# Performance work log

Measured on AMD Instinct MI355X. Metric: run time of the kernel, lower is better.

Reference implementation:

```python
import jax, jax.numpy as jnp
import numpy as np
from jax import lax

HEADS = 8
DK = 128
DV = 128  # attention_channels


def circ_conv(x, w):
    # Conv2d with circular padding that preserves spatial size (odd kernel).
    k = w.shape[2]
    p = k // 2
    if p > 0:
        x = jnp.pad(x, ((0, 0), (0, 0), (p, p), (p, p)), mode='wrap')
    return lax.conv_general_dilated(x, w, (1, 1), 'VALID',
                                    dimension_numbers=('NCHW', 'OIHW', 'NCHW'))


def setup_inputs() -> dict:
    key = jax.random.key(0)
    k1, k2, k3, k4 = jax.random.split(key, 4)
    x = jax.random.normal(k1, (4, 128, 48, 48), dtype=jnp.float32)
    w_init = jax.random.normal(k2, (128, 128, 3, 3), dtype=jnp.float32) * 0.03
    w_qkv = jax.random.normal(k3, (384, 128, 3, 3), dtype=jnp.float32) * 0.03
    w_out = jax.random.normal(k4, (128, 128, 1, 1), dtype=jnp.float32) * 0.1
    return {"x": x, "w_init": w_init, "w_qkv": w_qkv, "w_out": w_out}


def reference(x, w_init, w_qkv, w_out):
    out = circ_conv(x, w_init)               # (b, out_ch - dv, h, w)
    b, _, H, W = out.shape
    N = H * W
    dk_h = DK // HEADS
    dv_h = DV // HEADS

    qkv = circ_conv(x, w_qkv)                # (b, 2*dk+dv, h, w)
    q, k, v = jnp.split(qkv, [DK, 2 * DK], axis=1)

    scale = dk_h ** (-0.5)
    fq = q.reshape(b, HEADS, dk_h, N) * scale
    fk = k.reshape(b, HEADS, dk_h, N)
    fv = v.reshape(b, HEADS, dv_h, N)

    logits = jnp.einsum('bhdn,bhdm->bhnm', fq, fk)     # (b,H,N,N)
    weights = jax.nn.softmax(logits, axis=-1)
    attn = jnp.einsum('bhnm,bhdm->bhnd', weights, fv)  # (b,H,N,dv_h)

    # Faithful to torch: raw reshape (b,H,N,dv_h) -> (b,H,dv_h,h,w)
    attn = attn.reshape(b, HEADS, dv_h, H, W)
    attn = attn.reshape(b, HEADS * dv_h, H, W)
    attn = circ_conv(attn, w_out)
    return jnp.concatenate([out, attn], axis=1)
```

## Files before the change

### kernel.cpp

```cpp
#include <hip/hip_runtime.h>

typedef __attribute__((ext_vector_type(8))) short short8;
typedef __attribute__((ext_vector_type(4))) short shortx4;
typedef __attribute__((ext_vector_type(4))) float floatx4;
typedef __attribute__((ext_vector_type(4))) _Float16 half4;
typedef __attribute__((ext_vector_type(2))) _Float16 half2v;

__device__ __forceinline__ short bf16_short(float f) {
    unsigned u = __builtin_bit_cast(unsigned, f);
    u = (u + 0x7fff + ((u >> 16) & 1)) >> 16;
    return (short)u;
}

__device__ __forceinline__ float fast_exp2(float x) {
#if __has_builtin(__builtin_amdgcn_exp2f)
    return __builtin_amdgcn_exp2f(x);
#else
    return __expf(x * 0.6931471805599453f);
#endif
}

__device__ __forceinline__ half4 pk4(float p0, float p1, float p2, float p3) {
#if __has_builtin(__builtin_amdgcn_cvt_pkrtz)
    half2v lo = __builtin_bit_cast(half2v, __builtin_amdgcn_cvt_pkrtz(p0, p1));
    half2v hi = __builtin_bit_cast(half2v, __builtin_amdgcn_cvt_pkrtz(p2, p3));
    half4 o; o[0] = lo[0]; o[1] = lo[1]; o[2] = hi[0]; o[3] = hi[1];
    return o;
#else
    half4 o; o[0] = (_Float16)p0; o[1] = (_Float16)p1;
    o[2] = (_Float16)p2; o[3] = (_Float16)p3;
    return o;
#endif
}

__global__ __launch_bounds__(256) void transform_w(
    const float* __restrict__ wi, const float* __restrict__ wq,
    const float* __restrict__ wo, const float* __restrict__ x,
    short* __restrict__ Wt, short* __restrict__ Wot, short* __restrict__ Xt)
{
    if (blockIdx.x < 2368) {
        int idx = blockIdx.x * 256 + threadIdx.x;
        if (idx < 589824) {
            int j  = idx & 7;
            int t1 = idx >> 3;
            int co = t1 & 127;
            int t2 = t1 >> 7;
            int chunk = t2 & 15;
            int t3 = t2 >> 4;
            int cog = t3 & 3;
            int tap = t3 >> 2;
            int ci = chunk * 8 + j;
            float v;
            if (cog == 0) v = wi[(co * 128 + ci) * 9 + tap];
            else          v = wq[((((cog - 1) * 128) + co) * 128 + ci) * 9 + tap];
            Wt[idx] = bf16_short(v);
        } else {
            int i2 = idx - 589824;
            int j  = i2 & 7;
            int co = (i2 >> 3) & 127;
            int chunk = i2 >> 10;
            int ci = chunk * 8 + j;
            Wot[i2] = bf16_short(wo[co * 128 + ci]);
        }
    } else {
        int xid = (blockIdx.x - 2368) * 256 + threadIdx.x;
        int col   = xid % 48;
        int row   = (xid / 48) % 48;
        int chunk = (xid / 2304) % 16;
        int b     = xid / 36864;
        const float* xs = x + ((b * 128 + chunk * 8) * 48 + row) * 48 + col;
        short8 o;
        #pragma unroll
        for (int j = 0; j < 8; ++j) o[j] = bf16_short(xs[j * 2304]);
        *(short8*)&Xt[(size_t)xid * 8] = o;
    }
}

__global__ __launch_bounds__(256) void conv_main(
    const short* __restrict__ Xt, const short* __restrict__ Wt,
    float* __restrict__ dout, _Float16* __restrict__ qT,
    _Float16* __restrict__ kT, _Float16* __restrict__ vA)
{
    const int y   = blockIdx.x;
    const int cog = blockIdx.y;
    const int b   = blockIdx.z;

    __shared__ short Xs[16 * 3 * 48 * 8];

    const int t = threadIdx.x;
    const int wave = t >> 6, lane = t & 63, quad = lane >> 4, l16 = lane & 15;

    const short* wA = Wt + (size_t)cog * 16384 + (wave * 32 + l16) * 8;

    short8 A[2][8];
    #pragma unroll
    for (int kk = 0; kk < 4; ++kk) {
        int chA = kk * 4 + quad;
        A[0][kk * 2 + 0] = *(const short8*)(wA + chA * 1024);
        A[0][kk * 2 + 1] = *(const short8*)(wA + chA * 1024 + 128);
    }

    {
        const short* xtb = Xt + (size_t)b * 16 * 48 * 48 * 8;
        #pragma unroll
        for (int it = 0; it < 9; ++it) {
            int w     = it * 256 + t;
            int col   = w % 48;
            int row3  = (w / 48) % 3;
            int chunk = w / 144;
            int rowg  = y + row3 - 1;
            rowg = (rowg < 0) ? rowg + 48 : (rowg >= 48 ? rowg - 48 : rowg);
            short8 v = *(const short8*)&xtb[((chunk * 48 + rowg) * 48 + col) * 8];
            *(short8*)&Xs[((chunk * 3 + row3) * 48 + col) * 8] = v;
        }
    }

    floatx4 acc[2][3];
    #pragma unroll
    for (int i = 0; i < 2; ++i)
        #pragma unroll
        for (int jn = 0; jn < 3; ++jn) acc[i][jn] = (floatx4){0.f, 0.f, 0.f, 0.f};

    __syncthreads();

    #pragma unroll
    for (int tap = 0; tap < 9; ++tap) {
        const int cur = tap & 1;
        if (tap < 8) {
            const short* wn = wA + (tap + 1) * 65536;
            #pragma unroll
            for (int kk = 0; kk < 4; ++kk) {
                int chA = kk * 4 + quad;
                A[cur ^ 1][kk * 2 + 0] = *(const short8*)(wn + chA * 1024);
                A[cur ^ 1][kk * 2 + 1] = *(const short8*)(wn + chA * 1024 + 128);
            }
        }

        const int dy = tap / 3, dx = tap % 3;
        int colw[3];
        #pragma unroll
        for (int nt = 0; nt < 3; ++nt) {
            int c = nt * 16 + l16 + dx - 1;
            c = (c < 0) ? c + 48 : (c >= 48 ? c - 48 : c);
            colw[nt] = c;
        }

        #pragma unroll
        for (int kk = 0; kk < 4; ++kk) {
            int chA = kk * 4 + quad;
            short8 a0 = A[cur][kk * 2 + 0];
            short8 a1 = A[cur][kk * 2 + 1];
            #pragma unroll
            for (int nt = 0; nt < 3; ++nt) {
                short8 bf = *(const short8*)&Xs[((chA * 3 + dy) * 48 + colw[nt]) * 8];
                acc[0][nt] = __builtin_amdgcn_mfma_f32_16x16x32_bf16(a0, bf, acc[0][nt], 0, 0, 0);
                acc[1][nt] = __builtin_amdgcn_mfma_f32_16x16x32_bf16(a1, bf, acc[1][nt], 0, 0, 0);
            }
        }
    }

    if (cog == 0) {
        #pragma unroll
        for (int mt = 0; mt < 2; ++mt)
            #pragma unroll
            for (int nt = 0; nt < 3; ++nt)
                #pragma unroll
                for (int r = 0; r < 4; ++r) {
                    int n    = y * 48 + nt * 16 + l16;
                    int co_l = wave * 32 + mt * 16 + quad * 4 + r;
                    dout[(b * 256 + co_l) * 2304 + n] = acc[mt][nt][r];
                }
    } else if (cog == 3) {
        #pragma unroll
        for (int mt = 0; mt < 2; ++mt) {
            int hh = wave * 2 + mt;
            #pragma unroll
            for (int nt = 0; nt < 3; ++nt) {
                int s = y * 3 + nt;
                _Float16* dst = vA + (((size_t)(b * 8 + hh) * 144 + s) * 16) * 16 + l16;
                #pragma unroll
                for (int r = 0; r < 4; ++r)
                    dst[(quad * 4 + r) * 16] = (_Float16)acc[mt][nt][r];
            }
        }
    } else {
        _Float16* dst = (cog == 1) ? qT : kT;
        const float scale = (cog == 1) ? 0.360673762f : 1.0f;
        #pragma unroll
        for (int mt = 0; mt < 2; ++mt) {
            int hh = wave * 2 + mt;
            #pragma unroll
            for (int nt = 0; nt < 3; ++nt) {
                int n = y * 48 + nt * 16 + l16;
                half4 o;
                #pragma unroll
                for (int r = 0; r < 4; ++r) o[r] = (_Float16)(acc[mt][nt][r] * scale);
                *(half4*)&dst[((b * 8 + hh) * 2304 + n) * 16 + quad * 4] = o;
            }
        }
    }
}

__global__ __launch_bounds__(256) void attn_kernel(
    const _Float16* __restrict__ qT, const _Float16* __restrict__ kT,
    const _Float16* __restrict__ vA, short* __restrict__ attnbuf)
{
    const int bh = blockIdx.y;
    const int n0 = blockIdx.x * 64;

    __shared__ float Red[4][4][64][5];

    const int t = threadIdx.x;
    const int wave = t >> 6, lane = t & 63, quad = lane >> 4, l16 = lane & 15;

    const _Float16* qTb = qT + (size_t)bh * 2304 * 16;
    const _Float16* kTb = kT + (size_t)bh * 2304 * 16;
    const _Float16* vAb = vA + (size_t)bh * 144 * 256;

    half4 qf[4];
    #pragma unroll
    for (int f = 0; f < 4; ++f)
        qf[f] = *(const half4*)(qTb + (n0 + f * 16 + l16) * 16 + quad * 4);

    floatx4 accA[4], accB[4];
    float lsum[4];
    #pragma unroll
    for (int f = 0; f < 4; ++f) {
        accA[f] = (floatx4){0.f,0.f,0.f,0.f};
        accB[f] = (floatx4){0.f,0.f,0.f,0.f};
        lsum[f] = 0.f;
    }

    const int mbase = wave * 576;
    const int sig0  = wave * 36;
    const int vofs  = l16 * 16 + quad * 4;

    half4 kfA = *(const half4*)(kTb + (mbase + l16) * 16 + quad * 4);
    half4 vfA = *(const half4*)(vAb + sig0 * 256 + vofs);
    half4 kfB = *(const half4*)(kTb + (mbase + 16 + l16) * 16 + quad * 4);
    half4 vfB = *(const half4*)(vAb + (sig0 + 1) * 256 + vofs);

    #pragma unroll 2
    for (int s = 0; s < 18; ++s) {
        half4 kA = kfA, vAc = vfA, kB = kfB, vBc = vfB;
        if (s < 17) {
            int m1 = mbase + (s + 1) * 32;
            int sg = sig0 + (s + 1) * 2;
            kfA = *(const half4*)(kTb + (m1 + l16) * 16 + quad * 4);
            vfA = *(const half4*)(vAb + sg * 256 + vofs);
            kfB = *(const half4*)(kTb + (m1 + 16 + l16) * 16 + quad * 4);
            vfB = *(const half4*)(vAb + (sg + 1) * 256 + vofs);
        }
        floatx4 z = {0.f,0.f,0.f,0.f};
        floatx4 stA[4], stB[4];
        #pragma unroll
        for (int f = 0; f < 4; ++f)
            stA[f] = __builtin_amdgcn_mfma_f32_16x16x16f16(kA, qf[f], z, 0, 0, 0);
        #pragma unroll
        for (int f = 0; f < 4; ++f)
            stB[f] = __builtin_amdgcn_mfma_f32_16x16x16f16(kB, qf[f], z, 0, 0, 0);

        #pragma unroll
        for (int f = 0; f < 4; ++f) {
            float a0 = fast_exp2(stA[f][0]);
            float a1 = fast_exp2(stA[f][1]);
            float a2 = fast_exp2(stA[f][2]);
            float a3 = fast_exp2(stA[f][3]);
            lsum[f] += (a0 + a1) + (a2 + a3);
            accA[f] = __builtin_amdgcn_mfma_f32_16x16x16f16(vAc, pk4(a0,a1,a2,a3), accA[f], 0, 0, 0);
        }
        #pragma unroll
        for (int f = 0; f < 4; ++f) {
            float b0 = fast_exp2(stB[f][0]);
            float b1 = fast_exp2(stB[f][1]);
            float b2 = fast_exp2(stB[f][2]);
            float b3 = fast_exp2(stB[f][3]);
            lsum[f] += (b0 + b1) + (b2 + b3);
            accB[f] = __builtin_amdgcn_mfma_f32_16x16x16f16(vBc, pk4(b0,b1,b2,b3), accB[f], 0, 0, 0);
        }
    }

    #pragma unroll
    for (int f = 0; f < 4; ++f) {
        lsum[f] += __shfl_xor(lsum[f], 16, 64);
        lsum[f] += __shfl_xor(lsum[f], 32, 64);
    }

    #pragma unroll
    for (int f = 0; f < 4; ++f) {
        #pragma unroll
        for (int r = 0; r < 4; ++r) Red[wave][f][lane][r] = accA[f][r] + accB[f][r];
        Red[wave][f][lane][4] = lsum[f];
    }
    __syncthreads();

    {
        const int f = wave;
        float tot[4] = {0.f, 0.f, 0.f, 0.f};
        float ls = 0.f;
        #pragma unroll
        for (int w = 0; w < 4; ++w) {
            #pragma unroll
            for (int r = 0; r < 4; ++r) tot[r] += Red[w][f][lane][r];
            ls += Red[w][f][lane][4];
        }
        float rinv = 1.0f / ls;
        shortx4 o;
        #pragma unroll
        for (int r = 0; r < 4; ++r) o[r] = bf16_short(tot[r] * rinv);
        int n = n0 + f * 16 + l16;
        *(shortx4*)&attnbuf[((size_t)bh * 2304 + n) * 16 + quad * 4] = o;
    }
}

__global__ __launch_bounds__(256) void conv1x1(
    const short* __restrict__ attnbuf, const short* __restrict__ Wot,
    float* __restrict__ dout)
{
    const int b    = blockIdx.y;
    const int col0 = blockIdx.x * 32;
    constexpr int RSA = 136;

    __shared__ short Wo[16 * 128 * 8];
    __shared__ short As[32 * RSA];

    const int t = threadIdx.x;
    {
        short8* dst = (short8*)Wo;
        const short8* src = (const short8*)Wot;
        #pragma unroll
        for (int it = 0; it < 8; ++it) dst[it * 256 + t] = src[it * 256 + t];
    }
    {
        const short* ab = attnbuf + b * 128 * 2304;
        #pragma unroll
        for (int it = 0; it < 8; ++it) {
            int e = it * 256 + t;
            int ci = e >> 4, cp = e & 15;
            unsigned v = *(const unsigned*)(ab + ci * 2304 + col0 + cp * 2);
            As[(cp * 2) * RSA + ci]     = (short)(v & 0xffff);
            As[(cp * 2 + 1) * RSA + ci] = (short)(v >> 16);
        }
    }
    __syncthreads();

    const int wave = t >> 6, lane = t & 63, quad = lane >> 4, l16 = lane & 15;
    floatx4 acc[2][2];
    #pragma unroll
    for (int i = 0; i < 2; ++i)
        #pragma unroll
        for (int j = 0; j < 2; ++j) acc[i][j] = (floatx4){0.f, 0.f, 0.f, 0.f};

    #pragma unroll
    for (int kk = 0; kk < 4; ++kk) {
        int chA = kk * 4 + quad;
        short8 a0 = *(const short8*)&Wo[(chA * 128 + wave * 32 + l16) * 8];
        short8 a1 = *(const short8*)&Wo[(chA * 128 + wave * 32 + 16 + l16) * 8];
        #pragma unroll
        for (int nt = 0; nt < 2; ++nt) {
            short8 bf = *(const short8*)&As[(nt * 16 + l16) * RSA + kk * 32 + quad * 8];
            acc[0][nt] = __builtin_amdgcn_mfma_f32_16x16x32_bf16(a0, bf, acc[0][nt], 0, 0, 0);
            acc[1][nt] = __builtin_amdgcn_mfma_f32_16x16x32_bf16(a1, bf, acc[1][nt], 0, 0, 0);
        }
    }

    #pragma unroll
    for (int mt = 0; mt < 2; ++mt)
        #pragma unroll
        for (int nt = 0; nt < 2; ++nt)
            #pragma unroll
            for (int r = 0; r < 4; ++r) {
                int co  = wave * 32 + mt * 16 + quad * 4 + r;
                int col = col0 + nt * 16 + l16;
                dout[(b * 256 + 128 + co) * 2304 + col] = acc[mt][nt][r];
            }
}

extern "C" void kernel_launch(void* const* d_in, const int* in_sizes, int n_in,
                              void* d_out, int out_size, void* d_ws, size_t ws_size,
                              hipStream_t stream)
{
    const float* x  = (const float*)d_in[0];
    const float* wi = (const float*)d_in[1];
    const float* wq = (const float*)d_in[2];
    const float* wo = (const float*)d_in[3];
    float* dout = (float*)d_out;

    char* ws = (char*)d_ws;
    _Float16* qT   = (_Float16*)(ws);
    _Float16* kT   = (_Float16*)(ws + 2359296);
    _Float16* vA   = (_Float16*)(ws + 4718592);
    short* attnbuf = (short*)(ws + 7077888);
    short* Wt      = (short*)(ws + 9437184);
    short* Wot     = (short*)(ws + 10616832);
    short* Xt      = (short*)(ws + 10649600);

    transform_w<<<2944, 256, 0, stream>>>(wi, wq, wo, x, Wt, Wot, Xt);
    conv_main<<<dim3(48, 4, 4), 256, 0, stream>>>(Xt, Wt, dout, qT, kT, vA);
    attn_kernel<<<dim3(36, 32), 256, 0, stream>>>(qT, kT, vA, attnbuf);
    conv1x1<<<dim3(72, 4), 256, 0, stream>>>(attnbuf, Wot, dout);
}
```

Before: 121.5 us.

## Split conv K-reduction across two wave groups with LDS reduction

Doubles the conv_main block to 512 threads. Each half of the waves handles half of the input-channel chunks for every tap, and the partial accumulators are then summed through shared memory before the epilogue. The goal is more waves in flight per block and shorter per-wave MFMA chains, which should hide the weight-load latency better on a grid of only 768 blocks. In exchange it adds an LDS reduction with two extra barriers and leaves half the waves idle during the epilogue.

```diff
diff --git a/kernel.cpp b/kernel.cpp
--- a/kernel.cpp
+++ b/kernel.cpp
@@ -76,7 +76,7 @@
     }
 }
 
-__global__ __launch_bounds__(256) void conv_main(
+__global__ __launch_bounds__(512) void conv_main(
     const short* __restrict__ Xt, const short* __restrict__ Wt,
     float* __restrict__ dout, _Float16* __restrict__ qT,
     _Float16* __restrict__ kT, _Float16* __restrict__ vA)
@@ -89,13 +89,15 @@
 
     const int t = threadIdx.x;
     const int wave = t >> 6, lane = t & 63, quad = lane >> 4, l16 = lane & 15;
-
-    const short* wA = Wt + (size_t)cog * 16384 + (wave * 32 + l16) * 8;
-
-    short8 A[2][8];
-    #pragma unroll
-    for (int kk = 0; kk < 4; ++kk) {
-        int chA = kk * 4 + quad;
+    const int wv = wave & 3;
+    const int kk0 = (wave >> 2) * 2;
+
+    const short* wA = Wt + (size_t)cog * 16384 + (wv * 32 + l16) * 8;
+
+    short8 A[2][4];
+    #pragma unroll
+    for (int kk = 0; kk < 2; ++kk) {
+        int chA = (kk0 + kk) * 4 + quad;
         A[0][kk * 2 + 0] = *(const short8*)(wA + chA * 1024);
         A[0][kk * 2 + 1] = *(const short8*)(wA + chA * 1024 + 128);
     }
@@ -103,15 +105,17 @@
     {
         const short* xtb = Xt + (size_t)b * 16 * 48 * 48 * 8;
         #pragma unroll
-        for (int it = 0; it < 9; ++it) {
-            int w     = it * 256 + t;
-            int col   = w % 48;
-            int row3  = (w / 48) % 3;
-            int chunk = w / 144;
-            int rowg  = y + row3 - 1;
-            rowg = (rowg < 0) ? rowg + 48 : (rowg >= 48 ? rowg - 48 : rowg);
-            short8 v = *(const short8*)&xtb[((chunk * 48 + rowg) * 48 + col) * 8];
-            *(short8*)&Xs[((chunk * 3 + row3) * 48 + col) * 8] = v;
+        for (int it = 0; it < 5; ++it) {
+            int w = it * 512 + t;
+            if (w < 2304) {
+                int col   = w % 48;
+                int row3  = (w / 48) % 3;
+                int chunk = w / 144;
+                int rowg  = y + row3 - 1;
+                rowg = (rowg < 0) ? rowg + 48 : (rowg >= 48 ? rowg - 48 : rowg);
+                short8 v = *(const short8*)&xtb[((chunk * 48 + rowg) * 48 + col) * 8];
+                *(short8*)&Xs[((chunk * 3 + row3) * 48 + col) * 8] = v;
+            }
         }
     }
 
@@ -129,8 +133,8 @@
         if (tap < 8) {
             const short* wn = wA + (tap + 1) * 65536;
             #pragma unroll
-            for (int kk = 0; kk < 4; ++kk) {
-                int chA = kk * 4 + quad;
+            for (int kk = 0; kk < 2; ++kk) {
+                int chA = (kk0 + kk) * 4 + quad;
                 A[cur ^ 1][kk * 2 + 0] = *(const short8*)(wn + chA * 1024);
                 A[cur ^ 1][kk * 2 + 1] = *(const short8*)(wn + chA * 1024 + 128);
             }
@@ -146,8 +150,8 @@
         }
 
         #pragma unroll
-        for (int kk = 0; kk < 4; ++kk) {
-            int chA = kk * 4 + quad;
+        for (int kk = 0; kk < 2; ++kk) {
+            int chA = (kk0 + kk) * 4 + quad;
             short8 a0 = A[cur][kk * 2 + 0];
             short8 a1 = A[cur][kk * 2 + 1];
             #pragma unroll
@@ -157,6 +161,30 @@
                 acc[1][nt] = __builtin_amdgcn_mfma_f32_16x16x32_bf16(a1, bf, acc[1][nt], 0, 0, 0);
             }
         }
+    }
+
+    __syncthreads();
+    float* Rs = (float*)Xs;
+    if (wave >= 4) {
+        float* dst = Rs + ((wave - 4) * 64 + lane) * 25;
+        #pragma unroll
+        for (int mt = 0; mt < 2; ++mt)
+            #pragma unroll
+            for (int nt = 0; nt < 3; ++nt)
+                #pragma unroll
+                for (int r = 0; r < 4; ++r) dst[(mt * 3 + nt) * 4 + r] = acc[mt][nt][r];
+    }
+    __syncthreads();
+    if (wave >= 4) return;
+
+    {
+        const float* src = Rs + (wave * 64 + lane) * 25;
+        #pragma unroll
+        for (int mt = 0; mt < 2; ++mt)
+            #pragma unroll
+            for (int nt = 0; nt < 3; ++nt)
+                #pragma unroll
+                for (int r = 0; r < 4; ++r) acc[mt][nt][r] += src[(mt * 3 + nt) * 4 + r];
     }
 
     if (cog == 0) {
@@ -396,7 +424,7 @@
     short* Xt      = (short*)(ws + 10649600);
 
     transform_w<<<2944, 256, 0, stream>>>(wi, wq, wo, x, Wt, Wot, Xt);
-    conv_main<<<dim3(48, 4, 4), 256, 0, stream>>>(Xt, Wt, dout, qT, kT, vA);
+    conv_main<<<dim3(48, 4, 4), 512, 0, stream>>>(Xt, Wt, dout, qT, kT, vA);
     attn_kernel<<<dim3(36, 32), 256, 0, stream>>>(qT, kT, vA, attnbuf);
     conv1x1<<<dim3(72, 4), 256, 0, stream>>>(attnbuf, Wot, dout);
 }
```

Result: faster. 117.6 us (-3.2%).
